# Kernel optimization log

Measured on AMD Instinct MI355X. Metric: run time of the kernel, lower is better.

The kernel has to match this reference:

```python
import jax, jax.numpy as jnp
import numpy as np

B, N, D, H = 8, 1024, 1024, 16
DH = D // H
EPS = 1e-6


def setup_inputs() -> dict:
    key = jax.random.key(0)
    ks = jax.random.split(key, 12)
    s = 1.0 / np.sqrt(D)
    inp = {
        "x": jax.random.normal(ks[0], (B, N, D), jnp.float32),
        "y": jax.random.normal(ks[1], (B, N, D), jnp.float32),
        "Wq": jax.random.normal(ks[2], (D, D), jnp.float32) * s,
        "bq": jnp.zeros((D,), jnp.float32),
        "Wk": jax.random.normal(ks[3], (D, D), jnp.float32) * s,
        "bk": jnp.zeros((D,), jnp.float32),
        "Wv": jax.random.normal(ks[4], (D, D), jnp.float32) * s,
        "bv": jnp.zeros((D,), jnp.float32),
        "Wf": jax.random.normal(ks[5], (D, D), jnp.float32) * s,
        "bf": jnp.zeros((D,), jnp.float32),
        "g1": jnp.ones((D,), jnp.float32),
        "b1": jnp.zeros((D,), jnp.float32),
        "g2": jnp.ones((D,), jnp.float32),
        "b2": jnp.zeros((D,), jnp.float32),
    }
    return inp


def _layernorm(x, g, b):
    mu = jnp.mean(x, axis=-1, keepdims=True)
    var = jnp.mean(jnp.square(x - mu), axis=-1, keepdims=True)
    return (x - mu) * jax.lax.rsqrt(var + EPS) * g + b


def reference(x, y, Wq, bq, Wk, bk, Wv, bv, Wf, bf, g1, b1, g2, b2):
    q = x @ Wq + bq                      # [B, Nq, D]
    k = y @ Wk + bk                      # [B, Nk, D]
    v = y @ Wv + bv                      # [B, Nk, D]
    qh = q.reshape(B, N, H, DH)
    kh = k.reshape(B, N, H, DH)
    vh = v.reshape(B, N, H, DH)
    # NOTE: original scales by sqrt(embed_dim), not sqrt(head_dim)
    scores = jnp.einsum("bqhd,bkhd->bhqk", qh, kh) / jnp.sqrt(jnp.float32(D))
    att = jax.nn.softmax(scores, axis=-1)
    o = jnp.einsum("bhqk,bkhd->bqhd", att, vh).reshape(B, N, D)
    out = x + o
    out = _layernorm(out, g1, b1)
    out = out + jax.nn.relu(out @ Wf + bf)
    out = _layernorm(out, g2, b2)
    return out
```

## Files before the change

kernel.cpp:

```cpp
#include <hip/hip_runtime.h>


#define Bb 8
#define Nn 1024
#define Dd 1024
#define Hh 16
#define DH 64
#define Mrows (Bb * 1024)

#define QSCL 0.045084220027780106f

typedef float f32x4 __attribute__((ext_vector_type(4)));
typedef __bf16 bf16x8 __attribute__((ext_vector_type(8)));
typedef unsigned int u32x4 __attribute__((ext_vector_type(4)));

#define MFMA16(acc, a, b) \
  acc = __builtin_amdgcn_mfma_f32_16x16x32_bf16((a), (b), (acc), 0, 0, 0)

__device__ __forceinline__ bf16x8 ld_frag(const void* p) {
  u32x4 v = *(const u32x4*)p;
  return __builtin_bit_cast(bf16x8, v);
}

__device__ __forceinline__ void gload16(const void* g, void* l) {
  __builtin_amdgcn_global_load_lds(
      (const __attribute__((address_space(1))) unsigned int*)g,
      (__attribute__((address_space(3))) unsigned int*)l, 16, 0, 0);
}

__device__ __forceinline__ unsigned short f2bf(float f) {
  return __builtin_bit_cast(unsigned short, (__bf16)f);
}
__device__ __forceinline__ float bf2f(unsigned short s) {
  unsigned int u = ((unsigned int)s) << 16;
  return __builtin_bit_cast(float, u);
}
__device__ __forceinline__ unsigned cvt_pk_bf16(float a, float b) {
  unsigned r;
  asm("v_cvt_pk_bf16_f32 %0, %1, %2" : "=v"(r) : "v"(a), "v"(b));
  return r;
}

__global__ __launch_bounds__(256) void cvt_f32_bf16_2(
    const float* __restrict__ in0, unsigned short* __restrict__ out0,
    const float* __restrict__ in1, unsigned short* __restrict__ out1, int n4) {
  const float* in = blockIdx.y ? in1 : in0;
  unsigned short* out = blockIdx.y ? out1 : out0;
  int i = blockIdx.x * blockDim.x + threadIdx.x;
  int stride = gridDim.x * blockDim.x;
  for (; i < n4; i += stride) {
    float4 v = ((const float4*)in)[i];
    ushort4 o;
    o.x = f2bf(v.x); o.y = f2bf(v.y); o.z = f2bf(v.z); o.w = f2bf(v.w);
    ((ushort4*)out)[i] = o;
  }
}

__global__ __launch_bounds__(256) void transpose_cvt4(
    const float* __restrict__ W0, const float* __restrict__ W1,
    const float* __restrict__ W2, const float* __restrict__ W3,
    unsigned short* __restrict__ T0, unsigned short* __restrict__ T1,
    unsigned short* __restrict__ T2, unsigned short* __restrict__ T3) {
  __shared__ float tile[32][33];
  const float* W = blockIdx.z == 0 ? W0 : blockIdx.z == 1 ? W1
                   : blockIdx.z == 2 ? W2 : W3;
  unsigned short* Wt = blockIdx.z == 0 ? T0 : blockIdx.z == 1 ? T1
                       : blockIdx.z == 2 ? T2 : T3;
  int tx = threadIdx.x, ty = threadIdx.y;
  int n0 = blockIdx.x * 32, k0 = blockIdx.y * 32;
#pragma unroll
  for (int i = ty; i < 32; i += 8)
    tile[i][tx] = W[(size_t)(k0 + i) * Dd + n0 + tx];
  __syncthreads();
#pragma unroll
  for (int i = ty; i < 32; i += 8)
    Wt[(size_t)(n0 + i) * Dd + k0 + tx] = f2bf(tile[tx][i]);
}

struct GemmCtx { int m0, n0, wm, wn, lr, lk, lg, l, w; };

template <typename EpiFn>
__device__ __forceinline__ void gemm_core(
    const unsigned short* __restrict__ A, const unsigned short* __restrict__ Bt,
    int K, EpiFn epi) {
  __shared__ __attribute__((aligned(16))) unsigned short As[2][128 * 32];
  __shared__ __attribute__((aligned(16))) unsigned short Bs[2][128 * 32];
  const int bid = blockIdx.y * 8 + blockIdx.x;
  const int nwg = (gridDim.x * gridDim.y);
  const int swz = (bid & 7) * (nwg >> 3) + (bid >> 3);
  const int m0 = (swz >> 3) * 128, n0 = (swz & 7) * 128;
  const int t = threadIdx.x, w = t >> 6, l = t & 63;
  const int wm = (w >> 1) * 64, wn = (w & 1) * 64;
  const int lr = l & 15, lk = (l >> 4) * 8;
  const int rA = t >> 2, sA = (t & 3) * 8;
  char* AsB = (char*)As;
  char* BsB = (char*)Bs;
  const int wb = (w * 64) * 16;

  f32x4 acc[4][4] = {};

  for (int k0 = 0; k0 < K; k0 += 64) {
    __syncthreads();
#pragma unroll
    for (int h = 0; h < 2; ++h) {
      const int ko = k0 + h * 32;
      gload16(A + (size_t)(m0 + rA) * K + ko + sA, AsB + h * 8192 + wb);
      gload16(A + (size_t)(m0 + 64 + rA) * K + ko + sA, AsB + h * 8192 + wb + 4096);
      gload16(Bt + (size_t)(n0 + rA) * K + ko + sA, BsB + h * 8192 + wb);
      gload16(Bt + (size_t)(n0 + 64 + rA) * K + ko + sA, BsB + h * 8192 + wb + 4096);
    }
    __syncthreads();

#pragma unroll
    for (int h = 0; h < 2; ++h) {
      bf16x8 af[4], bfr[4];
#pragma unroll
      for (int i = 0; i < 4; ++i)
        af[i] = ld_frag(&As[h][(wm + i * 16 + lr) * 32 + lk]);
#pragma unroll
      for (int j = 0; j < 4; ++j)
        bfr[j] = ld_frag(&Bs[h][(wn + j * 16 + lr) * 32 + lk]);
#pragma unroll
      for (int i = 0; i < 4; ++i)
#pragma unroll
        for (int j = 0; j < 4; ++j) MFMA16(acc[i][j], af[i], bfr[j]);
    }
  }
  GemmCtx c{m0, n0, wm, wn, lr, lk, l >> 4, l, w};
  epi(acc, c);
}

__global__ __launch_bounds__(256) void gemm_qkv(
    const unsigned short* __restrict__ xb, const unsigned short* __restrict__ yb,
    const unsigned short* __restrict__ WqT, const unsigned short* __restrict__ WkT,
    const unsigned short* __restrict__ WvT,
    const float* __restrict__ bq, const float* __restrict__ bk,
    const float* __restrict__ bv,
    unsigned short* __restrict__ Qb, unsigned short* __restrict__ Kb,
    unsigned short* __restrict__ Vtb) {
  const int z = blockIdx.z;
  const unsigned short* A = (z == 0) ? xb : yb;
  const unsigned short* Bt = (z == 0) ? WqT : (z == 1) ? WkT : WvT;
  const float* bias = (z == 0) ? bq : (z == 1) ? bk : bv;
  unsigned short* Cb = (z == 0) ? Qb : Kb;

  gemm_core(A, Bt, Dd, [&](f32x4 (&acc)[4][4], GemmCtx c) {
#pragma unroll
    for (int i = 0; i < 4; ++i)
#pragma unroll
      for (int j = 0; j < 4; ++j) {
        int col = c.n0 + c.wn + j * 16 + c.lr;
        float bcol = bias[col];
        if (z == 2) {
          int brow = c.m0 + c.wm + i * 16 + c.lg * 4;
          int bi = brow >> 10, nloc = brow & 1023;
          int nperm = (nloc & ~31) | (((nloc >> 2) & 3) << 3) |
                      (((nloc >> 4) & 1) << 2);
          ushort4 o4;
          o4.x = f2bf(acc[i][j][0] + bcol);
          o4.y = f2bf(acc[i][j][1] + bcol);
          o4.z = f2bf(acc[i][j][2] + bcol);
          o4.w = f2bf(acc[i][j][3] + bcol);
          *(ushort4*)(Vtb + ((size_t)bi * Dd + col) * Nn + nperm) = o4;
        } else {
          float scl = (z == 0) ? QSCL : 1.0f;
#pragma unroll
          for (int r = 0; r < 4; ++r) {
            int row = c.m0 + c.wm + i * 16 + c.lg * 4 + r;
            Cb[(size_t)row * Dd + col] = f2bf((acc[i][j][r] + bcol) * scl);
          }
        }
      }
  });
}

__global__ __launch_bounds__(256) void gemm_ff(
    const unsigned short* __restrict__ A, const unsigned short* __restrict__ Bt,
    const float* __restrict__ bias, const unsigned short* __restrict__ Tres,
    unsigned short* __restrict__ Cb) {
  gemm_core(A, Bt, Dd, [&](f32x4 (&acc)[4][4], GemmCtx c) {
#pragma unroll
    for (int i = 0; i < 4; ++i)
#pragma unroll
      for (int j = 0; j < 4; ++j) {
        int col = c.n0 + c.wn + j * 16 + c.lr;
        float bcol = bias[col];
#pragma unroll
        for (int r = 0; r < 4; ++r) {
          int row = c.m0 + c.wm + i * 16 + c.lg * 4 + r;
          size_t idx = (size_t)row * Dd + col;
          Cb[idx] = f2bf(bf2f(Tres[idx]) + fmaxf(acc[i][j][r] + bcol, 0.f));
        }
      }
  });
}

__global__ __launch_bounds__(256) void attn_fwd(
    const unsigned short* __restrict__ Qg, const unsigned short* __restrict__ Kg,
    const unsigned short* __restrict__ Vt, unsigned short* __restrict__ Obf) {
  __shared__ __attribute__((aligned(16))) unsigned short Ks[64 * 64];
  __shared__ __attribute__((aligned(16))) unsigned short Vts[64 * 64];
  char* KsB = (char*)Ks;
  char* VtsB = (char*)Vts;

  const int bid = blockIdx.y * 8 + blockIdx.x;
  const int swz = (bid & 7) * 128 + (bid >> 3);
  const int q0 = (swz & 7) * 128;
  const int by = swz >> 3;
  const int b = by >> 4, h = by & 15;

  const int t = threadIdx.x, w = t >> 6, l = t & 63;
  const int lr = l & 15, lg = l >> 4;

  bf16x8 aq[2][2];
#pragma unroll
  for (int i = 0; i < 2; ++i) {
    const unsigned short* qp =
        Qg + ((size_t)b * Nn + q0 + w * 32 + i * 16 + lr) * Dd + h * DH + lg * 8;
    aq[i][0] = *(const bf16x8*)qp;
    aq[i][1] = *(const bf16x8*)(qp + 32);
  }

  u32x4 one4 = {0x3F803F80u, 0x3F803F80u, 0x3F803F80u, 0x3F803F80u};
  const bf16x8 vones = __builtin_bit_cast(bf16x8, one4);

  const size_t baseK = (size_t)b * Nn * Dd + h * DH;
  const size_t baseV = ((size_t)b * Dd + h * DH) * Nn;

  const int srow = t >> 3, sch = t & 7;
  const int sby = srow * 128 + ((sch * 16) ^ ((srow & 7) << 4));
  const int sby2 = sby + 32 * 128;

  uint4 kA = *(const uint4*)(Kg + baseK + (size_t)srow * Dd + sch * 8);
  uint4 kB = *(const uint4*)(Kg + baseK + (size_t)(srow + 32) * Dd + sch * 8);
  uint4 vA = *(const uint4*)(Vt + baseV + (size_t)srow * Nn + sch * 8);
  uint4 vB = *(const uint4*)(Vt + baseV + (size_t)(srow + 32) * Nn + sch * 8);

  f32x4 oacc[4][2] = {};
  f32x4 lacc[2] = {};

  for (int kv = 0; kv < Nn / 64; ++kv) {
    __syncthreads();
    *(uint4*)(KsB + sby) = kA;
    *(uint4*)(KsB + sby2) = kB;
    *(uint4*)(VtsB + sby) = vA;
    *(uint4*)(VtsB + sby2) = vB;
    __syncthreads();

    if (kv + 1 < Nn / 64) {
      int kvo = (kv + 1) * 64;
      kA = *(const uint4*)(Kg + baseK + (size_t)(kvo + srow) * Dd + sch * 8);
      kB = *(const uint4*)(Kg + baseK + (size_t)(kvo + srow + 32) * Dd + sch * 8);
      vA = *(const uint4*)(Vt + baseV + (size_t)srow * Nn + kvo + sch * 8);
      vB = *(const uint4*)(Vt + baseV + (size_t)(srow + 32) * Nn + kvo + sch * 8);
    }

    f32x4 st[2][4];
    __builtin_amdgcn_s_setprio(1);
#pragma unroll
    for (int j = 0; j < 4; ++j) {
      const int kro = (j * 16 + lr) * 128;
      const int ksw = ((lg ^ ((lr & 7))) << 4);
      bf16x8 k0 = ld_frag(KsB + kro + (((lg ^ (lr & 7))) << 4));
      bf16x8 k1 = ld_frag(KsB + kro + ((((lg + 4) ^ (lr & 7))) << 4));
#pragma unroll
      for (int i = 0; i < 2; ++i) {
        f32x4 z = {0.f, 0.f, 0.f, 0.f};
        MFMA16(z, k0, aq[i][0]);
        MFMA16(z, k1, aq[i][1]);
        st[i][j] = z;
      }
    }
    __builtin_amdgcn_s_setprio(0);

#pragma unroll
    for (int i = 0; i < 2; ++i)
#pragma unroll
      for (int j = 0; j < 4; ++j) {
        st[i][j][0] = exp2f(st[i][j][0]);
        st[i][j][1] = exp2f(st[i][j][1]);
        st[i][j][2] = exp2f(st[i][j][2]);
        st[i][j][3] = exp2f(st[i][j][3]);
      }

#pragma unroll
    for (int m = 0; m < 2; ++m) {
      bf16x8 pb[2];
#pragma unroll
      for (int i = 0; i < 2; ++i) {
        u32x4 pk;
        pk[0] = cvt_pk_bf16(st[i][2 * m][0], st[i][2 * m][1]);
        pk[1] = cvt_pk_bf16(st[i][2 * m][2], st[i][2 * m][3]);
        pk[2] = cvt_pk_bf16(st[i][2 * m + 1][0], st[i][2 * m + 1][1]);
        pk[3] = cvt_pk_bf16(st[i][2 * m + 1][2], st[i][2 * m + 1][3]);
        pb[i] = __builtin_bit_cast(bf16x8, pk);
      }
      __builtin_amdgcn_s_setprio(1);
      MFMA16(lacc[0], vones, pb[0]);
      MFMA16(lacc[1], vones, pb[1]);
#pragma unroll
      for (int da = 0; da < 4; ++da) {
        const int vrow = da * 16 + lr;
        bf16x8 va = ld_frag(
            VtsB + vrow * 128 + (((lg + 4 * m) ^ (vrow & 7)) << 4));
        MFMA16(oacc[da][0], va, pb[0]);
        MFMA16(oacc[da][1], va, pb[1]);
      }
      __builtin_amdgcn_s_setprio(0);
    }
  }

#pragma unroll
  for (int i = 0; i < 2; ++i) {
    float rd = 1.f / lacc[i][0];
    const size_t orow = (size_t)b * Nn + q0 + w * 32 + i * 16 + lr;
#pragma unroll
    for (int da = 0; da < 4; ++da) {
      ushort4 o4;
      o4.x = f2bf(oacc[da][i][0] * rd);
      o4.y = f2bf(oacc[da][i][1] * rd);
      o4.z = f2bf(oacc[da][i][2] * rd);
      o4.w = f2bf(oacc[da][i][3] * rd);
      *(ushort4*)(Obf + orow * Dd + h * DH + da * 16 + lg * 4) = o4;
    }
  }
}

template <int MODE>
__global__ __launch_bounds__(256) void ln_k(
    const unsigned short* __restrict__ X, const unsigned short* __restrict__ Oin,
    const float* __restrict__ gamma, const float* __restrict__ beta,
    unsigned short* __restrict__ out_bf, float* __restrict__ out_f) {
  __shared__ float red[8];
  const int row = blockIdx.x, t = threadIdx.x;
  ushort4 xu = ((const ushort4*)(X + (size_t)row * Dd))[t];
  float4 v = {bf2f(xu.x), bf2f(xu.y), bf2f(xu.z), bf2f(xu.w)};
  if (MODE == 0) {
    ushort4 o = ((const ushort4*)(Oin + (size_t)row * Dd))[t];
    v.x += bf2f(o.x); v.y += bf2f(o.y); v.z += bf2f(o.z); v.w += bf2f(o.w);
  }
  float s = v.x + v.y + v.z + v.w;
#pragma unroll
  for (int o = 32; o > 0; o >>= 1) s += __shfl_xor(s, o, 64);
  if ((t & 63) == 0) red[t >> 6] = s;
  __syncthreads();
  float mean = (red[0] + red[1] + red[2] + red[3]) * (1.f / 1024.f);
  float dx = v.x - mean, dy = v.y - mean, dz = v.z - mean, dw = v.w - mean;
  float s2 = dx * dx + dy * dy + dz * dz + dw * dw;
#pragma unroll
  for (int o = 32; o > 0; o >>= 1) s2 += __shfl_xor(s2, o, 64);
  if ((t & 63) == 0) red[4 + (t >> 6)] = s2;
  __syncthreads();
  float var = (red[4] + red[5] + red[6] + red[7]) * (1.f / 1024.f);
  float rstd = rsqrtf(var + 1e-6f);
  float4 g = ((const float4*)gamma)[t];
  float4 bb = ((const float4*)beta)[t];
  float r0 = dx * rstd * g.x + bb.x;
  float r1 = dy * rstd * g.y + bb.y;
  float r2 = dz * rstd * g.z + bb.z;
  float r3 = dw * rstd * g.w + bb.w;
  if (MODE == 0) {
    ushort4 o4;
    o4.x = f2bf(r0); o4.y = f2bf(r1); o4.z = f2bf(r2); o4.w = f2bf(r3);
    ((ushort4*)(out_bf + (size_t)row * Dd))[t] = o4;
  } else {
    float4 o4 = {r0, r1, r2, r3};
    ((float4*)(out_f + (size_t)row * Dd))[t] = o4;
  }
}

extern "C" void kernel_launch(void* const* d_in, const int* in_sizes, int n_in,
                              void* d_out, int out_size, void* d_ws, size_t ws_size,
                              hipStream_t stream) {
  const float* x  = (const float*)d_in[0];
  const float* y  = (const float*)d_in[1];
  const float* Wq = (const float*)d_in[2];
  const float* bq = (const float*)d_in[3];
  const float* Wk = (const float*)d_in[4];
  const float* bk = (const float*)d_in[5];
  const float* Wv = (const float*)d_in[6];
  const float* bv = (const float*)d_in[7];
  const float* Wf = (const float*)d_in[8];
  const float* bf = (const float*)d_in[9];
  const float* g1 = (const float*)d_in[10];
  const float* b1 = (const float*)d_in[11];
  const float* g2 = (const float*)d_in[12];
  const float* b2 = (const float*)d_in[13];

  char* ws = (char*)d_ws;
  const size_t MB = 1024 * 1024;
  unsigned short* xb  = (unsigned short*)(ws + 0 * MB);
  unsigned short* yb  = (unsigned short*)(ws + 16 * MB);
  unsigned short* WqT = (unsigned short*)(ws + 32 * MB);
  unsigned short* WkT = (unsigned short*)(ws + 34 * MB);
  unsigned short* WvT = (unsigned short*)(ws + 36 * MB);
  unsigned short* WfT = (unsigned short*)(ws + 38 * MB);
  unsigned short* Qb  = (unsigned short*)(ws + 40 * MB);
  unsigned short* Kb  = (unsigned short*)(ws + 56 * MB);
  unsigned short* Vtb = (unsigned short*)(ws + 72 * MB);
  unsigned short* Obf = (unsigned short*)(ws + 16 * MB);
  unsigned short* tb  = (unsigned short*)(ws + 40 * MB);
  unsigned short* ub  = (unsigned short*)(ws + 56 * MB);

  const int n4 = (Mrows * Dd) / 4;
  cvt_f32_bf16_2<<<dim3(1024, 2), 256, 0, stream>>>(x, xb, y, yb, n4);

  transpose_cvt4<<<dim3(32, 32, 4), dim3(32, 8), 0, stream>>>(
      Wq, Wk, Wv, Wf, WqT, WkT, WvT, WfT);

  gemm_qkv<<<dim3(8, 64, 3), 256, 0, stream>>>(
      xb, yb, WqT, WkT, WvT, bq, bk, bv, Qb, Kb, Vtb);

  attn_fwd<<<dim3(8, 128), 256, 0, stream>>>(Qb, Kb, Vtb, Obf);

  ln_k<0><<<Mrows, 256, 0, stream>>>(xb, Obf, g1, b1, tb, nullptr);

  gemm_ff<<<dim3(8, 64), 256, 0, stream>>>(tb, WfT, bf, tb, ub);

  ln_k<1><<<Mrows, 256, 0, stream>>>(ub, nullptr, g2, b2, nullptr, (float*)d_out);
}
```

Measured before the change: 208.3 us.

## Merge prep kernels and double-buffer K/V in 512-thread attention blocks

Folds the input bf16 conversion and the weight transpose-convert into one launch, removing a kernel launch. Attention now uses 512-thread blocks covering 256 queries, so each K/V tile staged in LDS is shared by twice as many waves. The K/V tile is double-buffered, which leaves one barrier per iteration instead of two and lets the global loads overlap the MFMA work. The cost is more LDS per block and fewer, larger workgroups, which could lower occupancy.

Measured after the change: 195.9 us. 6.0% less time.

```diff
diff --git a/kernel.cpp b/kernel.cpp
--- a/kernel.cpp
+++ b/kernel.cpp
@@ -41,40 +41,40 @@
   return r;
 }
 
-__global__ __launch_bounds__(256) void cvt_f32_bf16_2(
-    const float* __restrict__ in0, unsigned short* __restrict__ out0,
-    const float* __restrict__ in1, unsigned short* __restrict__ out1, int n4) {
-  const float* in = blockIdx.y ? in1 : in0;
-  unsigned short* out = blockIdx.y ? out1 : out0;
-  int i = blockIdx.x * blockDim.x + threadIdx.x;
-  int stride = gridDim.x * blockDim.x;
-  for (; i < n4; i += stride) {
-    float4 v = ((const float4*)in)[i];
-    ushort4 o;
-    o.x = f2bf(v.x); o.y = f2bf(v.y); o.z = f2bf(v.z); o.w = f2bf(v.w);
-    ((ushort4*)out)[i] = o;
-  }
-}
-
-__global__ __launch_bounds__(256) void transpose_cvt4(
+__global__ __launch_bounds__(256) void prep(
+    const float* __restrict__ x, const float* __restrict__ y,
+    unsigned short* __restrict__ xb, unsigned short* __restrict__ yb,
     const float* __restrict__ W0, const float* __restrict__ W1,
     const float* __restrict__ W2, const float* __restrict__ W3,
     unsigned short* __restrict__ T0, unsigned short* __restrict__ T1,
     unsigned short* __restrict__ T2, unsigned short* __restrict__ T3) {
   __shared__ float tile[32][33];
-  const float* W = blockIdx.z == 0 ? W0 : blockIdx.z == 1 ? W1
-                   : blockIdx.z == 2 ? W2 : W3;
-  unsigned short* Wt = blockIdx.z == 0 ? T0 : blockIdx.z == 1 ? T1
-                       : blockIdx.z == 2 ? T2 : T3;
-  int tx = threadIdx.x, ty = threadIdx.y;
-  int n0 = blockIdx.x * 32, k0 = blockIdx.y * 32;
-#pragma unroll
-  for (int i = ty; i < 32; i += 8)
-    tile[i][tx] = W[(size_t)(k0 + i) * Dd + n0 + tx];
-  __syncthreads();
-#pragma unroll
-  for (int i = ty; i < 32; i += 8)
-    Wt[(size_t)(n0 + i) * Dd + k0 + tx] = f2bf(tile[tx][i]);
+  const int z = blockIdx.z, t = threadIdx.x;
+  if (z < 2) {
+    const float* in = z ? y : x;
+    unsigned short* out = z ? yb : xb;
+    const int n4 = (Mrows * Dd) / 4;
+    int i = blockIdx.x * 256 + t;
+    int stride = 1024 * 256;
+    for (; i < n4; i += stride) {
+      float4 v = ((const float4*)in)[i];
+      ushort4 o;
+      o.x = f2bf(v.x); o.y = f2bf(v.y); o.z = f2bf(v.z); o.w = f2bf(v.w);
+      ((ushort4*)out)[i] = o;
+    }
+  } else {
+    const float* W = z == 2 ? W0 : z == 3 ? W1 : z == 4 ? W2 : W3;
+    unsigned short* Wt = z == 2 ? T0 : z == 3 ? T1 : z == 4 ? T2 : T3;
+    const int tx = t & 31, ty = t >> 5;
+    const int n0 = (blockIdx.x & 31) * 32, k0 = (blockIdx.x >> 5) * 32;
+#pragma unroll
+    for (int i = ty; i < 32; i += 8)
+      tile[i][tx] = W[(size_t)(k0 + i) * Dd + n0 + tx];
+    __syncthreads();
+#pragma unroll
+    for (int i = ty; i < 32; i += 8)
+      Wt[(size_t)(n0 + i) * Dd + k0 + tx] = f2bf(tile[tx][i]);
+  }
 }
 
 struct GemmCtx { int m0, n0, wm, wn, lr, lk, lg, l, w; };
@@ -195,18 +195,16 @@
   });
 }
 
-__global__ __launch_bounds__(256) void attn_fwd(
+__global__ __launch_bounds__(512) void attn_fwd(
     const unsigned short* __restrict__ Qg, const unsigned short* __restrict__ Kg,
     const unsigned short* __restrict__ Vt, unsigned short* __restrict__ Obf) {
-  __shared__ __attribute__((aligned(16))) unsigned short Ks[64 * 64];
-  __shared__ __attribute__((aligned(16))) unsigned short Vts[64 * 64];
-  char* KsB = (char*)Ks;
-  char* VtsB = (char*)Vts;
-
-  const int bid = blockIdx.y * 8 + blockIdx.x;
-  const int swz = (bid & 7) * 128 + (bid >> 3);
-  const int q0 = (swz & 7) * 128;
-  const int by = swz >> 3;
+  __shared__ __attribute__((aligned(16))) unsigned short KVs[2][2][64 * 64];
+  char* lbase = (char*)KVs;
+
+  const int bid = blockIdx.y * 4 + blockIdx.x;
+  const int swz = (bid & 7) * 64 + (bid >> 3);
+  const int q0 = (swz & 3) * 256;
+  const int by = swz >> 2;
   const int b = by >> 4, h = by & 15;
 
   const int t = threadIdx.x, w = t >> 6, l = t & 63;
@@ -229,30 +227,25 @@
 
   const int srow = t >> 3, sch = t & 7;
   const int sby = srow * 128 + ((sch * 16) ^ ((srow & 7) << 4));
-  const int sby2 = sby + 32 * 128;
 
   uint4 kA = *(const uint4*)(Kg + baseK + (size_t)srow * Dd + sch * 8);
-  uint4 kB = *(const uint4*)(Kg + baseK + (size_t)(srow + 32) * Dd + sch * 8);
   uint4 vA = *(const uint4*)(Vt + baseV + (size_t)srow * Nn + sch * 8);
-  uint4 vB = *(const uint4*)(Vt + baseV + (size_t)(srow + 32) * Nn + sch * 8);
+
+  *(uint4*)(lbase + sby) = kA;
+  *(uint4*)(lbase + 8192 + sby) = vA;
+  __syncthreads();
 
   f32x4 oacc[4][2] = {};
   f32x4 lacc[2] = {};
 
   for (int kv = 0; kv < Nn / 64; ++kv) {
-    __syncthreads();
-    *(uint4*)(KsB + sby) = kA;
-    *(uint4*)(KsB + sby2) = kB;
-    *(uint4*)(VtsB + sby) = vA;
-    *(uint4*)(VtsB + sby2) = vB;
-    __syncthreads();
-
-    if (kv + 1 < Nn / 64) {
+    char* kcur = lbase + (kv & 1) * 16384;
+    char* vcur = kcur + 8192;
+    const bool more = (kv + 1) < Nn / 64;
+    if (more) {
       int kvo = (kv + 1) * 64;
       kA = *(const uint4*)(Kg + baseK + (size_t)(kvo + srow) * Dd + sch * 8);
-      kB = *(const uint4*)(Kg + baseK + (size_t)(kvo + srow + 32) * Dd + sch * 8);
       vA = *(const uint4*)(Vt + baseV + (size_t)srow * Nn + kvo + sch * 8);
-      vB = *(const uint4*)(Vt + baseV + (size_t)(srow + 32) * Nn + kvo + sch * 8);
     }
 
     f32x4 st[2][4];
@@ -260,9 +253,8 @@
 #pragma unroll
     for (int j = 0; j < 4; ++j) {
       const int kro = (j * 16 + lr) * 128;
-      const int ksw = ((lg ^ ((lr & 7))) << 4);
-      bf16x8 k0 = ld_frag(KsB + kro + (((lg ^ (lr & 7))) << 4));
-      bf16x8 k1 = ld_frag(KsB + kro + ((((lg + 4) ^ (lr & 7))) << 4));
+      bf16x8 k0 = ld_frag(kcur + kro + (((lg ^ (lr & 7))) << 4));
+      bf16x8 k1 = ld_frag(kcur + kro + ((((lg + 4) ^ (lr & 7))) << 4));
 #pragma unroll
       for (int i = 0; i < 2; ++i) {
         f32x4 z = {0.f, 0.f, 0.f, 0.f};
@@ -302,11 +294,18 @@
       for (int da = 0; da < 4; ++da) {
         const int vrow = da * 16 + lr;
         bf16x8 va = ld_frag(
-            VtsB + vrow * 128 + (((lg + 4 * m) ^ (vrow & 7)) << 4));
+            vcur + vrow * 128 + (((lg + 4 * m) ^ (vrow & 7)) << 4));
         MFMA16(oacc[da][0], va, pb[0]);
         MFMA16(oacc[da][1], va, pb[1]);
       }
       __builtin_amdgcn_s_setprio(0);
+    }
+
+    if (more) {
+      char* knxt = lbase + ((kv + 1) & 1) * 16384;
+      *(uint4*)(knxt + sby) = kA;
+      *(uint4*)(knxt + 8192 + sby) = vA;
+      __syncthreads();
     }
   }
 
@@ -402,16 +401,13 @@
   unsigned short* tb  = (unsigned short*)(ws + 40 * MB);
   unsigned short* ub  = (unsigned short*)(ws + 56 * MB);
 
-  const int n4 = (Mrows * Dd) / 4;
-  cvt_f32_bf16_2<<<dim3(1024, 2), 256, 0, stream>>>(x, xb, y, yb, n4);
-
-  transpose_cvt4<<<dim3(32, 32, 4), dim3(32, 8), 0, stream>>>(
-      Wq, Wk, Wv, Wf, WqT, WkT, WvT, WfT);
+  prep<<<dim3(1024, 1, 6), 256, 0, stream>>>(
+      x, y, xb, yb, Wq, Wk, Wv, Wf, WqT, WkT, WvT, WfT);
 
   gemm_qkv<<<dim3(8, 64, 3), 256, 0, stream>>>(
       xb, yb, WqT, WkT, WvT, bq, bk, bv, Qb, Kb, Vtb);
 
-  attn_fwd<<<dim3(8, 128), 256, 0, stream>>>(Qb, Kb, Vtb, Obf);
+  attn_fwd<<<dim3(4, 128), 512, 0, stream>>>(Qb, Kb, Vtb, Obf);
 
   ln_k<0><<<Mrows, 256, 0, stream>>>(xb, Obf, g1, b1, tb, nullptr);
 
```
